# Optimization experiments

Measured on AMD Instinct MI355X. Metric: run time of the kernel, lower is better.

## Reference

```python
import jax, jax.numpy as jnp
import numpy as np

WS = 14  # window size
NH = 12  # num heads
EPS = 1e-5  # torch LayerNorm eps


def _rel_idx(ws: int) -> np.ndarray:
    coords = np.stack(np.meshgrid(np.arange(ws), np.arange(ws), indexing='ij'))
    cf = coords.reshape(2, -1)                      # (2, N)
    rel = cf[:, :, None] - cf[:, None, :]           # (2, N, N)
    rel = rel.transpose(1, 2, 0).copy()
    rel[:, :, 0] += ws - 1
    rel[:, :, 1] += ws - 1
    rel[:, :, 0] *= 2 * ws - 1
    return rel.sum(-1)                              # (N, N) int


def _layernorm(x, w, b):
    mu = jnp.mean(x, axis=-1, keepdims=True)
    var = jnp.var(x, axis=-1, keepdims=True)
    return (x - mu) * jax.lax.rsqrt(var + EPS) * w + b


def setup_inputs() -> dict:
    key = jax.random.key(0)
    ks = jax.random.split(key, 8)
    d, dff = 768, 3072
    s = lambda k, shape, sc: jax.random.normal(k, shape, jnp.float32) * sc
    return {
        'x': jax.random.normal(ks[0], (8, d, 56, 56), jnp.float32),
        'norm1_w': jnp.ones((d,), jnp.float32),
        'norm1_b': jnp.zeros((d,), jnp.float32),
        'qkv_w': s(ks[1], (d, 3 * d), 0.02),
        'qkv_b': jnp.zeros((3 * d,), jnp.float32),
        'rel_bias_table': s(ks[2], ((2 * WS - 1) ** 2, NH), 0.02),
        'proj_w': s(ks[3], (d, d), 0.02),
        'proj_b': jnp.zeros((d,), jnp.float32),
        'norm2_w': jnp.ones((d,), jnp.float32),
        'norm2_b': jnp.zeros((d,), jnp.float32),
        'fc1_w': s(ks[4], (d, dff), 0.02),
        'fc1_b': jnp.zeros((dff,), jnp.float32),
        'fc2_w': s(ks[5], (dff, d), 0.02),
        'fc2_b': jnp.zeros((d,), jnp.float32),
        'gamma1': jnp.full((d,), 1e-5, jnp.float32),
        'gamma2': jnp.full((d,), 1e-5, jnp.float32),
    }


def reference(x, norm1_w, norm1_b, qkv_w, qkv_b, rel_bias_table, proj_w, proj_b,
              norm2_w, norm2_b, fc1_w, fc1_b, fc2_w, fc2_b, gamma1, gamma2):
    B, C, H, W = x.shape
    nh, hd = NH, C // NH
    N = WS * WS
    xs = jnp.transpose(x, (0, 2, 3, 1))             # B,H,W,C
    shortcut = xs
    h = _layernorm(xs, norm1_w, norm1_b)

    # window partition (H, W divisible by WS)
    hw = h.reshape(B, H // WS, WS, W // WS, WS, C)
    hw = jnp.transpose(hw, (0, 1, 3, 2, 4, 5)).reshape(-1, N, C)  # (Bw, N, C)

    qkv = hw @ qkv_w + qkv_b                        # (Bw, N, 3C)
    qkv = qkv.reshape(-1, N, 3, nh, hd)
    q, k, v = [jnp.transpose(qkv[:, :, i], (0, 2, 1, 3)) for i in range(3)]  # (Bw,nh,N,hd)

    attn = jnp.einsum('bhnd,bhmd->bhnm', q, k) * (hd ** -0.5)
    rel_idx = jnp.asarray(_rel_idx(WS))             # static (N,N)
    bias = rel_bias_table[rel_idx]                  # (N,N,nh)
    attn = attn + jnp.transpose(bias, (2, 0, 1))[None]
    attn = jax.nn.softmax(attn, axis=-1)

    out = jnp.einsum('bhnm,bhmd->bnhd', attn, v).reshape(-1, N, C)
    out = out @ proj_w + proj_b                     # (Bw, N, C)

    # window reverse
    out = out.reshape(B, H // WS, W // WS, WS, WS, C)
    out = jnp.transpose(out, (0, 1, 3, 2, 4, 5)).reshape(B, H, W, C)

    xs = shortcut + gamma1 * out
    h2 = _layernorm(xs, norm2_w, norm2_b)
    mlp = jax.nn.gelu(h2 @ fc1_w + fc1_b, approximate=False) @ fc2_w + fc2_b
    xs = xs + gamma2 * mlp
    return jnp.transpose(xs, (0, 3, 1, 2))          # B,C,H,W
```

## Files before the change

### kernel.cpp

```cpp
#include <hip/hip_runtime.h>
#include <cstdint>
#include <cstddef>


typedef unsigned short u16;
typedef short short8 __attribute__((ext_vector_type(8)));
typedef float floatx4 __attribute__((ext_vector_type(4)));

static __device__ __forceinline__ float bf2f(u16 u) {
  return __uint_as_float(((unsigned)u) << 16);
}
static __device__ __forceinline__ u16 f2bf(float f) {
  unsigned u = __float_as_uint(f);
  return (u16)((u + 0x7FFFu + ((u >> 16) & 1u)) >> 16);
}
static __device__ __forceinline__ float ldin(const void* p, size_t i, int isf) {
  return isf ? ((const float*)p)[i] : bf2f(((const u16*)p)[i]);
}
static __device__ __forceinline__ void gload_lds16(const void* g, void* l) {
  __builtin_amdgcn_global_load_lds(
      (const __attribute__((address_space(1))) void*)g,
      (__attribute__((address_space(3))) void*)l, 16, 0, 0);
}
static __device__ __forceinline__ float fast_gelu(float v) {
  float u2 = v * (1.5957691216f + 0.0713548163f * v * v);
  return v * (1.0f / (1.0f + __expf(-u2)));
}

__global__ __launch_bounds__(256) void detect_kernel(const u16* __restrict__ x,
                                                     int* __restrict__ flag) {
  __shared__ int tot;
  if (threadIdx.x == 0) tot = 0;
  __syncthreads();
  int cnt = 0;
  for (int i = threadIdx.x; i < 4096; i += 256) {
    int e = (x[i] >> 7) & 0xFF;
    if (e >= 0xC1) cnt++;
  }
  atomicAdd(&tot, cnt);
  __syncthreads();
  if (threadIdx.x == 0) flag[0] = (tot > 16) ? 1 : 0;
}

__global__ __launch_bounds__(256) void cvt_params_kernel(
    const void* n1w, const void* n1b, const void* qkvb, const void* projb,
    const void* n2w, const void* n2b, const void* fc1b, const void* fc2b,
    const void* g1, const void* g2, const void* bt, u16* __restrict__ P,
    const int* __restrict__ flag) {
  int isf = *flag;
  int i = blockIdx.x * 256 + threadIdx.x;
  const void* src; int off;
  if      (i < 768)   { src = n1w;   off = i; }
  else if (i < 1536)  { src = n1b;   off = i - 768; }
  else if (i < 3840)  { src = qkvb;  off = i - 1536; }
  else if (i < 4608)  { src = projb; off = i - 3840; }
  else if (i < 5376)  { src = n2w;   off = i - 4608; }
  else if (i < 6144)  { src = n2b;   off = i - 5376; }
  else if (i < 9216)  { src = fc1b;  off = i - 6144; }
  else if (i < 9984)  { src = fc2b;  off = i - 9216; }
  else if (i < 10752) { src = g1;    off = i - 9984; }
  else if (i < 11520) { src = g2;    off = i - 10752; }
  else if (i < 20268) { src = bt;    off = i - 11520; }
  else return;
  P[i] = f2bf(ldin(src, off, isf));
}

__global__ __launch_bounds__(256) void wtr_kernel(const void* __restrict__ W,
                                                  u16* __restrict__ WT,
                                                  int K, int N,
                                                  const int* __restrict__ flag) {
  int isf = *flag;
  __shared__ u16 tl[32][33];
  int tx = threadIdx.x, ty = threadIdx.y;
  int n0 = blockIdx.x * 32, k0 = blockIdx.y * 32;
#pragma unroll
  for (int j = 0; j < 32; j += 8)
    tl[ty + j][tx] = f2bf(ldin(W, (size_t)(k0 + ty + j) * N + n0 + tx, isf));
  __syncthreads();
#pragma unroll
  for (int j = 0; j < 32; j += 8)
    WT[(size_t)(n0 + ty + j) * K + k0 + tx] = tl[tx][ty + j];
}

__global__ __launch_bounds__(256) void tin_kernel(const void* __restrict__ x,
                                                  u16* __restrict__ sc,
                                                  const int* __restrict__ flag) {
  int isf = *flag;
  int cc = blockIdx.x, h = blockIdx.y, b = blockIdx.z;
  __shared__ u16 tile[64 * 57];
  int tid = threadIdx.x;
  for (int i = tid; i < 64 * 56; i += 256) {
    int ci = i / 56, w = i - ci * 56;
    tile[ci * 57 + w] =
        f2bf(ldin(x, (((size_t)b * 768 + cc * 64 + ci) * 56 + h) * 56 + w, isf));
  }
  __syncthreads();
  int hb = h / 14, hi = h - hb * 14;
  for (int i = tid; i < 56 * 64; i += 256) {
    int w = i >> 6, ci = i & 63;
    int wb = w / 14, wj = w - wb * 14;
    int r = (b * 16 + hb * 4 + wb) * 196 + hi * 14 + wj;
    sc[(size_t)r * 768 + cc * 64 + ci] = tile[ci * 57 + w];
  }
}

__global__ __launch_bounds__(256) void tout_kernel(const u16* __restrict__ src,
                                                   void* __restrict__ out,
                                                   const int* __restrict__ flag) {
  int isf = *flag;
  int cc = blockIdx.x, h = blockIdx.y, b = blockIdx.z;
  __shared__ u16 tile[64 * 57];
  int tid = threadIdx.x;
  int hb = h / 14, hi = h - hb * 14;
  for (int i = tid; i < 56 * 64; i += 256) {
    int w = i >> 6, ci = i & 63;
    int wb = w / 14, wj = w - wb * 14;
    int r = (b * 16 + hb * 4 + wb) * 196 + hi * 14 + wj;
    tile[ci * 57 + w] = src[(size_t)r * 768 + cc * 64 + ci];
  }
  __syncthreads();
  for (int i = tid; i < 64 * 56; i += 256) {
    int ci = i / 56, w = i - ci * 56;
    size_t o = (((size_t)b * 768 + cc * 64 + ci) * 56 + h) * 56 + w;
    if (isf) ((float*)out)[o] = bf2f(tile[ci * 57 + w]);
    else     ((u16*)out)[o]   = tile[ci * 57 + w];
  }
}

__global__ __launch_bounds__(256) void ln_kernel(const u16* __restrict__ xin,
                                                 const u16* __restrict__ wt,
                                                 const u16* __restrict__ bs,
                                                 u16* __restrict__ out) {
  int row = blockIdx.x, t = threadIdx.x;
  const u16* xr = xin + (size_t)row * 768;
  float v0 = bf2f(xr[t]), v1 = bf2f(xr[t + 256]), v2 = bf2f(xr[t + 512]);
  float s1 = v0 + v1 + v2;
  float s2 = v0 * v0 + v1 * v1 + v2 * v2;
#pragma unroll
  for (int off = 32; off > 0; off >>= 1) {
    s1 += __shfl_xor(s1, off);
    s2 += __shfl_xor(s2, off);
  }
  __shared__ float p1[4], p2[4];
  if ((t & 63) == 0) { p1[t >> 6] = s1; p2[t >> 6] = s2; }
  __syncthreads();
  float S1 = p1[0] + p1[1] + p1[2] + p1[3];
  float S2 = p2[0] + p2[1] + p2[2] + p2[3];
  float mu = S1 * (1.f / 768.f);
  float var = S2 * (1.f / 768.f) - mu * mu;
  float rs = rsqrtf(var + 1e-5f);
  u16* orow = out + (size_t)row * 768;
  orow[t]       = f2bf((v0 - mu) * rs * bf2f(wt[t])       + bf2f(bs[t]));
  orow[t + 256] = f2bf((v1 - mu) * rs * bf2f(wt[t + 256]) + bf2f(bs[t + 256]));
  orow[t + 512] = f2bf((v2 - mu) * rs * bf2f(wt[t + 512]) + bf2f(bs[t + 512]));
}

template <int EPI, int NPH>
__global__ __launch_bounds__(512, 2) void gemm256_kernel(
    const u16* __restrict__ A, const u16* __restrict__ BT,
    const u16* __restrict__ bias, const u16* __restrict__ gamma,
    u16* __restrict__ out, int M, int N, int K, int NX, int NYT) {
  constexpr int BN  = 64 * NPH;
  constexpr int WM  = 8 / NPH;
  constexpr int MF  = 2 * NPH;
  constexpr int ATS = 16384;
  constexpr int BTS = 4096 * NPH;
  __shared__ __align__(16) u16 LDS[2 * ATS + 2 * BTS];

  int bid = blockIdx.x;
  int r8 = bid & 7, q = bid >> 3;
  int xb = q % NX, yb = (q / NX) * 8 + r8;
  if (yb >= NYT) return;
  int m0 = yb * 256, n0 = xb * BN;

  int tid = threadIdx.x;
  int w = tid >> 6, l = tid & 63;
  int l15 = l & 15, quad = l >> 4;
  int wm = w & (WM - 1), wn = w / WM;

  int lrow8 = l >> 3;
  int lk = ((l & 7) ^ lrow8) * 8;
  const u16* aptr[4];
  const u16* bptr[NPH];
#pragma unroll
  for (int j = 0; j < 4; ++j) {
    int ra = m0 + w * 32 + j * 8 + lrow8;
    if (ra > M - 1) ra = M - 1;
    aptr[j] = A + (size_t)ra * K + lk;
  }
#pragma unroll
  for (int j = 0; j < NPH; ++j) {
    int rb = n0 + (w * NPH + j) * 8 + lrow8;
    bptr[j] = BT + (size_t)rb * K + lk;
  }
  int kq0 = (((quad * 16)      ^ ((l15 & 7) << 4)) >> 1);
  int kq1 = (((64 + quad * 16) ^ ((l15 & 7) << 4)) >> 1);

  floatx4 acc[MF][4];
#pragma unroll
  for (int i = 0; i < MF; ++i)
#pragma unroll
    for (int jn = 0; jn < 4; ++jn)
#pragma unroll
      for (int e = 0; e < 4; ++e) acc[i][jn][e] = 0.f;

  int nt = K >> 6;
#pragma unroll
  for (int j = 0; j < 4; ++j)
    gload_lds16(aptr[j], LDS + (w * 4 + j) * 512);
#pragma unroll
  for (int j = 0; j < NPH; ++j)
    gload_lds16(bptr[j], LDS + 2 * ATS + (w * NPH + j) * 512);

  for (int t = 0; t < nt; ++t) {
    int cur = t & 1, nxt = cur ^ 1;
    const u16* Ac = LDS + cur * ATS;
    const u16* Bc = LDS + 2 * ATS + cur * BTS;
    u16* An = LDS + nxt * ATS;
    u16* Bn = LDS + 2 * ATS + nxt * BTS;
    bool pf = (t + 1) < nt;
    int ko = (t + 1) << 6;
    asm volatile("s_waitcnt vmcnt(0)" ::: "memory");
    __builtin_amdgcn_s_barrier();
    short8 bfr[4][2];
#pragma unroll
    for (int p = 0; p < NPH; ++p) {
      if (p == 0) {
#pragma unroll
        for (int ni = 0; ni < 4; ++ni) {
          const u16* bp = Bc + (wn * 64 + ni * 16 + l15) * 64;
          bfr[ni][0] = *(const short8*)(bp + kq0);
          bfr[ni][1] = *(const short8*)(bp + kq1);
        }
      }
      short8 af0[2], af1[2];
      {
        const u16* ap0 = Ac + (wm * (32 * NPH) + (2 * p) * 16 + l15) * 64;
        const u16* ap1 = ap0 + 16 * 64;
        af0[0] = *(const short8*)(ap0 + kq0);
        af0[1] = *(const short8*)(ap0 + kq1);
        af1[0] = *(const short8*)(ap1 + kq0);
        af1[1] = *(const short8*)(ap1 + kq1);
      }
      if (pf) {
        if constexpr (NPH == 4) {
          gload_lds16(aptr[p] + ko, An + (w * 4 + p) * 512);
          gload_lds16(bptr[p] + ko, Bn + (w * 4 + p) * 512);
        } else {
          gload_lds16(aptr[2 * p] + ko,     An + (w * 4 + 2 * p) * 512);
          gload_lds16(aptr[2 * p + 1] + ko, An + (w * 4 + 2 * p + 1) * 512);
          gload_lds16(bptr[p] + ko,         Bn + (w * 2 + p) * 512);
        }
      }
      __builtin_amdgcn_s_barrier();
      __builtin_amdgcn_s_setprio(1);
#pragma unroll
      for (int ni = 0; ni < 4; ++ni) {
        acc[2 * p][ni] = __builtin_amdgcn_mfma_f32_16x16x32_bf16(
            af0[0], bfr[ni][0], acc[2 * p][ni], 0, 0, 0);
        acc[2 * p][ni] = __builtin_amdgcn_mfma_f32_16x16x32_bf16(
            af0[1], bfr[ni][1], acc[2 * p][ni], 0, 0, 0);
        acc[2 * p + 1][ni] = __builtin_amdgcn_mfma_f32_16x16x32_bf16(
            af1[0], bfr[ni][0], acc[2 * p + 1][ni], 0, 0, 0);
        acc[2 * p + 1][ni] = __builtin_amdgcn_mfma_f32_16x16x32_bf16(
            af1[1], bfr[ni][1], acc[2 * p + 1][ni], 0, 0, 0);
      }
      __builtin_amdgcn_s_setprio(0);
      __builtin_amdgcn_s_barrier();
    }
  }

  constexpr int CSTR = BN + 8;
  u16* Cs = LDS;
  float bv[4];
#pragma unroll
  for (int ni = 0; ni < 4; ++ni)
    bv[ni] = bf2f(bias[n0 + wn * 64 + ni * 16 + l15]);
  for (int cch = 0; cch < 2; ++cch) {
    __syncthreads();
    if (((wm * NPH) >> 2) == cch) {
      int rbase = wm * (32 * NPH) - cch * 128 + quad * 4;
#pragma unroll
      for (int mi = 0; mi < MF; ++mi)
#pragma unroll
        for (int ni = 0; ni < 4; ++ni) {
          int cl = wn * 64 + ni * 16 + l15;
#pragma unroll
          for (int reg = 0; reg < 4; ++reg) {
            float v = acc[mi][ni][reg] + bv[ni];
            if constexpr (EPI == 2) v = fast_gelu(v);
            Cs[(rbase + mi * 16 + reg) * CSTR + cl] = f2bf(v);
          }
        }
    }
    __syncthreads();
#pragma unroll
    for (int it = 0; it < BN / 32; ++it) {
      int idx = it * 512 + tid;
      int row = idx / (BN / 8);
      int c8 = (idx - row * (BN / 8)) * 8;
      int grow = m0 + cch * 128 + row;
      if (grow < M) {
        short8 val = *(const short8*)&Cs[row * CSTR + c8];
        u16* po = out + (size_t)grow * N + n0 + c8;
        if constexpr (EPI == 1) {
          short8 rv = *(const short8*)po;
          short8 gv = *(const short8*)(gamma + n0 + c8);
          short8 res;
#pragma unroll
          for (int e = 0; e < 8; ++e)
            res[e] = (short)f2bf(bf2f((u16)rv[e]) +
                                 bf2f((u16)gv[e]) * bf2f((u16)val[e]));
          *(short8*)po = res;
        } else {
          *(short8*)po = val;
        }
      }
    }
  }
}

__global__ __launch_bounds__(256) void attn_kernel(const u16* __restrict__ qkv,
                                                   const u16* __restrict__ btab,
                                                   u16* __restrict__ out) {
  __shared__ __align__(16) u16 VT[64 * 232];
  __shared__ __align__(16) u16 Pa[4 * 2 * 512];
  __shared__ float bS[729];
  int bid = blockIdx.x;
  int win = bid / 12, h = bid - win * 12;
  int tid = threadIdx.x, w = tid >> 6, l = tid & 63;
  int lane15 = l & 15, quad = l >> 4;
  const u16* qbase = qkv + (size_t)win * 196 * 2304;

  for (int i = tid; i < 64 * 28; i += 256) {
    int d = i / 28, m = i - d * 28;
    VT[d * 232 + 196 + m] = 0;
  }
  for (int i = tid; i < 196 * 64; i += 256) {
    int m = i >> 6, d = i & 63;
    VT[d * 232 + m] = qbase[(size_t)m * 2304 + 1536 + h * 64 + d];
  }
  for (int i = tid; i < 729; i += 256) bS[i] = bf2f(btab[i * 12 + h]);
  __syncthreads();

  u16* Pw = Pa + w * 1024;
  for (int rt = w; rt < 13; rt += 4) {
    floatx4 acc[13];
#pragma unroll
    for (int nt = 0; nt < 13; ++nt)
#pragma unroll
      for (int e = 0; e < 4; ++e) acc[nt][e] = 0.f;

    int rq = rt * 16 + lane15;
    bool qok = rq < 196;
#pragma unroll
    for (int kk = 0; kk < 2; ++kk) {
      short8 qf;
      if (qok)
        qf = *(const short8*)&qbase[(size_t)rq * 2304 + h * 64 + kk * 32 + quad * 8];
      else
#pragma unroll
        for (int e = 0; e < 8; ++e) qf[e] = 0;
#pragma unroll
      for (int nt = 0; nt < 13; ++nt) {
        int n = nt * 16 + lane15;
        short8 kf = *(const short8*)&qbase[(size_t)n * 2304 + 768 + h * 64 + kk * 32 + quad * 8];
        acc[nt] = __builtin_amdgcn_mfma_f32_16x16x32_bf16(qf, kf, acc[nt], 0, 0, 0);
      }
    }

    int i1[4], j1[4]; bool rv[4]; float mx[4], sm[4];
#pragma unroll
    for (int reg = 0; reg < 4; ++reg) {
      int r = rt * 16 + quad * 4 + reg;
      i1[reg] = r / 14; j1[reg] = r - i1[reg] * 14;
      rv[reg] = r < 196; mx[reg] = -1e30f; sm[reg] = 0.f;
    }
#pragma unroll
    for (int nt = 0; nt < 13; ++nt) {
      int cc = nt * 16 + lane15;
      bool cv = cc < 196;
      int i2 = cc / 14, j2 = cc - i2 * 14;
#pragma unroll
      for (int reg = 0; reg < 4; ++reg) {
        float v;
        if (cv) {
          v = acc[nt][reg] * 0.125f;
          if (rv[reg]) v += bS[(i1[reg] - i2 + 13) * 27 + (j1[reg] - j2 + 13)];
        } else v = -1e30f;
        acc[nt][reg] = v;
        mx[reg] = fmaxf(mx[reg], v);
      }
    }
#pragma unroll
    for (int reg = 0; reg < 4; ++reg)
#pragma unroll
      for (int off = 1; off < 16; off <<= 1)
        mx[reg] = fmaxf(mx[reg], __shfl_xor(mx[reg], off));
#pragma unroll
    for (int nt = 0; nt < 13; ++nt)
#pragma unroll
      for (int reg = 0; reg < 4; ++reg) {
        float p = __expf(acc[nt][reg] - mx[reg]);
        acc[nt][reg] = p; sm[reg] += p;
      }
#pragma unroll
    for (int reg = 0; reg < 4; ++reg) {
#pragma unroll
      for (int off = 1; off < 16; off <<= 1) sm[reg] += __shfl_xor(sm[reg], off);
      sm[reg] = 1.f / sm[reg];
    }

    floatx4 oa[4];
#pragma unroll
    for (int dt = 0; dt < 4; ++dt)
#pragma unroll
      for (int e = 0; e < 4; ++e) oa[dt][e] = 0.f;
#pragma unroll
    for (int kk = 0; kk < 7; ++kk) {
      u16* Pb = Pw + (kk & 1) * 512;
#pragma unroll
      for (int p = 0; p < 2; ++p) {
        int nt = kk * 2 + p;
#pragma unroll
        for (int reg = 0; reg < 4; ++reg) {
          float v = (nt < 13) ? acc[nt][reg] * sm[reg] : 0.f;
          Pb[(quad * 4 + reg) * 32 + p * 16 + lane15] = f2bf(v);
        }
      }
      asm volatile("s_waitcnt lgkmcnt(0)" ::: "memory");
      short8 pf = *(const short8*)&Pb[lane15 * 32 + quad * 8];
#pragma unroll
      for (int dt = 0; dt < 4; ++dt) {
        short8 vf = *(const short8*)&VT[(dt * 16 + lane15) * 232 + kk * 32 + quad * 8];
        oa[dt] = __builtin_amdgcn_mfma_f32_16x16x32_bf16(pf, vf, oa[dt], 0, 0, 0);
      }
    }
#pragma unroll
    for (int dt = 0; dt < 4; ++dt)
#pragma unroll
      for (int reg = 0; reg < 4; ++reg) {
        int r = rt * 16 + quad * 4 + reg;
        if (r < 196)
          out[((size_t)win * 196 + r) * 768 + h * 64 + dt * 16 + lane15] =
              f2bf(oa[dt][reg]);
      }
  }
}

static inline int gemm_grid(int NX, int NYT) { return NX * ((NYT + 7) / 8) * 8; }

extern "C" void kernel_launch(void* const* d_in, const int* in_sizes, int n_in,
                              void* d_out, int out_size, void* d_ws, size_t ws_size,
                              hipStream_t stream) {
  const void* x      = d_in[0];
  const void* n1w    = d_in[1];
  const void* n1b    = d_in[2];
  const void* qkv_w  = d_in[3];
  const void* qkv_b  = d_in[4];
  const void* btab   = d_in[5];
  const void* proj_w = d_in[6];
  const void* proj_b = d_in[7];
  const void* n2w    = d_in[8];
  const void* n2b    = d_in[9];
  const void* fc1_w  = d_in[10];
  const void* fc1_b  = d_in[11];
  const void* fc2_w  = d_in[12];
  const void* fc2_b  = d_in[13];
  const void* gamma1 = d_in[14];
  const void* gamma2 = d_in[15];
  (void)in_sizes; (void)n_in; (void)out_size;

  int c;
  if      (ws_size >= 245432576ull) c = 1;
  else if (ws_size >= 168362240ull) c = 2;
  else                              c = 4;
  const int R = 25088 / c;
  const int WN = 128 / c;
  const int NYT = (R + 255) / 256;

  char* ws = (char*)d_ws;
  int*  flag  = (int*)ws;
  u16*  P     = (u16*)(ws + 256);
  u16*  qkvT  = (u16*)(ws + 65792);
  u16*  projT = (u16*)(ws + 65792 + 3538944);
  u16*  fc1T  = (u16*)(ws + 65792 + 4718592);
  u16*  fc2T  = (u16*)(ws + 65792 + 9437184);
  const size_t B0 = 38535168;
  u16*  buf0  = (u16*)(ws + 14221568);
  u16*  buf1  = (u16*)(ws + 14221568 + B0);
  char* scr   = ws + 14221568 + 2 * B0;

  u16 *p_n1w = P, *p_n1b = P + 768, *p_qkvb = P + 1536, *p_projb = P + 3840;
  u16 *p_n2w = P + 4608, *p_n2b = P + 5376, *p_fc1b = P + 6144;
  u16 *p_fc2b = P + 9216, *p_g1 = P + 9984, *p_g2 = P + 10752, *p_bt = P + 11520;

  dim3 b256(256), b512(512), bw(32, 8);
  detect_kernel<<<dim3(1), b256, 0, stream>>>((const u16*)x, flag);
  cvt_params_kernel<<<dim3(80), b256, 0, stream>>>(
      n1w, n1b, qkv_b, proj_b, n2w, n2b, fc1_b, fc2_b, gamma1, gamma2, btab,
      P, flag);
  wtr_kernel<<<dim3(72, 24), bw, 0, stream>>>(qkv_w, qkvT, 768, 2304, flag);
  wtr_kernel<<<dim3(24, 24), bw, 0, stream>>>(proj_w, projT, 768, 768, flag);
  wtr_kernel<<<dim3(96, 24), bw, 0, stream>>>(fc1_w, fc1T, 768, 3072, flag);
  wtr_kernel<<<dim3(24, 96), bw, 0, stream>>>(fc2_w, fc2T, 3072, 768, flag);

  tin_kernel<<<dim3(12, 56, 8), b256, 0, stream>>>(x, buf0, flag);
  ln_kernel<<<dim3(25088), b256, 0, stream>>>(buf0, p_n1w, p_n1b, buf1);

  for (int hc = 0; hc < c; ++hc) {
    size_t ro = (size_t)hc * R * 768;
    u16* qC = (u16*)scr;
    u16* aC = (u16*)(scr + (size_t)R * 4608);
    gemm256_kernel<0, 4><<<dim3(gemm_grid(9, NYT)), b512, 0, stream>>>(
        buf1 + ro, qkvT, p_qkvb, nullptr, qC, R, 2304, 768, 9, NYT);
    attn_kernel<<<dim3(WN * 12), b256, 0, stream>>>(qC, p_bt, aC);
    gemm256_kernel<1, 2><<<dim3(gemm_grid(6, NYT)), b512, 0, stream>>>(
        aC, projT, p_projb, p_g1, buf0 + ro, R, 768, 768, 6, NYT);
  }

  ln_kernel<<<dim3(25088), b256, 0, stream>>>(buf0, p_n2w, p_n2b, buf1);

  for (int hc = 0; hc < c; ++hc) {
    size_t ro = (size_t)hc * R * 768;
    u16* gC = (u16*)scr;
    gemm256_kernel<2, 4><<<dim3(gemm_grid(12, NYT)), b512, 0, stream>>>(
        buf1 + ro, fc1T, p_fc1b, nullptr, gC, R, 3072, 768, 12, NYT);
    gemm256_kernel<1, 2><<<dim3(gemm_grid(6, NYT)), b512, 0, stream>>>(
        gC, fc2T, p_fc2b, p_g2, buf0 + ro, R, 768, 3072, 6, NYT);
  }

  tout_kernel<<<dim3(12, 56, 8), b256, 0, stream>>>(buf0, d_out, flag);
}
```

Baseline: 996.4 us.

## Switch GEMM mainloop to 4-stage BK=32 LDS pipeline with partial vmcnt waits

Restructures the 256-row GEMM main loop from a double-buffered BK=64 scheme to a four-buffer ring with BK=32 tiles, prefetching three stages ahead with direct global-to-LDS loads. It waits with partial vmcnt counts instead of draining all outstanding loads, uses one barrier per k-step instead of several, and changes the LDS swizzle to match the narrower tile. The aim is to hide global memory latency better and cut synchronisation overhead. In exchange, each MFMA burst per barrier is smaller and the loop runs twice as many iterations.

```diff
diff --git a/kernel.cpp b/kernel.cpp
--- a/kernel.cpp
+++ b/kernel.cpp
@@ -160,12 +160,13 @@
     const u16* __restrict__ A, const u16* __restrict__ BT,
     const u16* __restrict__ bias, const u16* __restrict__ gamma,
     u16* __restrict__ out, int M, int N, int K, int NX, int NYT) {
-  constexpr int BN  = 64 * NPH;
-  constexpr int WM  = 8 / NPH;
-  constexpr int MF  = 2 * NPH;
-  constexpr int ATS = 16384;
-  constexpr int BTS = 4096 * NPH;
-  __shared__ __align__(16) u16 LDS[2 * ATS + 2 * BTS];
+  constexpr int BN   = 64 * NPH;
+  constexpr int WM   = 8 / NPH;
+  constexpr int MF   = 2 * NPH;
+  constexpr int ABUF = 8192;
+  constexpr int BBUF = 2048 * NPH;
+  constexpr int BUFSZ = ABUF + BBUF;
+  __shared__ __align__(16) u16 LDS[4 * BUFSZ];
 
   int bid = blockIdx.x;
   int r8 = bid & 7, q = bid >> 3;
@@ -178,23 +179,26 @@
   int l15 = l & 15, quad = l >> 4;
   int wm = w & (WM - 1), wn = w / WM;
 
-  int lrow8 = l >> 3;
-  int lk = ((l & 7) ^ lrow8) * 8;
-  const u16* aptr[4];
-  const u16* bptr[NPH];
-#pragma unroll
-  for (int j = 0; j < 4; ++j) {
-    int ra = m0 + w * 32 + j * 8 + lrow8;
-    if (ra > M - 1) ra = M - 1;
-    aptr[j] = A + (size_t)ra * K + lk;
-  }
-#pragma unroll
-  for (int j = 0; j < NPH; ++j) {
-    int rb = n0 + (w * NPH + j) * 8 + lrow8;
-    bptr[j] = BT + (size_t)rb * K + lk;
-  }
-  int kq0 = (((quad * 16)      ^ ((l15 & 7) << 4)) >> 1);
-  int kq1 = (((64 + quad * 16) ^ ((l15 & 7) << 4)) >> 1);
+  int lrow16 = l >> 2;
+  int lk = ((l & 3) ^ ((l >> 3) & 3)) * 8;
+  int ra0 = m0 + w * 32 + lrow16;       if (ra0 > M - 1) ra0 = M - 1;
+  int ra1 = m0 + w * 32 + 16 + lrow16;  if (ra1 > M - 1) ra1 = M - 1;
+  const u16* a0 = A + (size_t)ra0 * K + lk;
+  const u16* a1 = A + (size_t)ra1 * K + lk;
+  const u16* b0;
+  const u16* b1;
+  int dB0, dB1;
+  if constexpr (NPH == 4) {
+    b0 = BT + (size_t)(n0 + w * 32 + lrow16) * K + lk;
+    b1 = BT + (size_t)(n0 + w * 32 + 16 + lrow16) * K + lk;
+    dB0 = (w * 2) * 512; dB1 = (w * 2 + 1) * 512;
+  } else {
+    b0 = BT + (size_t)(n0 + w * 16 + lrow16) * K + lk;
+    b1 = b0; dB0 = w * 512; dB1 = 0;
+  }
+  int dA0 = (w * 2) * 512, dA1 = (w * 2 + 1) * 512;
+
+  int kqs = (quad ^ ((l15 >> 1) & 3)) * 8;
 
   floatx4 acc[MF][4];
 #pragma unroll
@@ -204,70 +208,52 @@
 #pragma unroll
       for (int e = 0; e < 4; ++e) acc[i][jn][e] = 0.f;
 
-  int nt = K >> 6;
-#pragma unroll
-  for (int j = 0; j < 4; ++j)
-    gload_lds16(aptr[j], LDS + (w * 4 + j) * 512);
-#pragma unroll
-  for (int j = 0; j < NPH; ++j)
-    gload_lds16(bptr[j], LDS + 2 * ATS + (w * NPH + j) * 512);
+  int nt = K >> 5;
+
+  auto STAGE = [&](int s) {
+    u16* bb = LDS + (size_t)(s & 3) * BUFSZ;
+    int ko = s << 5;
+    gload_lds16(a0 + ko, bb + dA0);
+    gload_lds16(a1 + ko, bb + dA1);
+    gload_lds16(b0 + ko, bb + ABUF + dB0);
+    if constexpr (NPH == 4) gload_lds16(b1 + ko, bb + ABUF + dB1);
+  };
+
+#pragma unroll
+  for (int pt = 0; pt < 3; ++pt)
+    if (pt < nt) STAGE(pt);
 
   for (int t = 0; t < nt; ++t) {
-    int cur = t & 1, nxt = cur ^ 1;
-    const u16* Ac = LDS + cur * ATS;
-    const u16* Bc = LDS + 2 * ATS + cur * BTS;
-    u16* An = LDS + nxt * ATS;
-    u16* Bn = LDS + 2 * ATS + nxt * BTS;
-    bool pf = (t + 1) < nt;
-    int ko = (t + 1) << 6;
-    asm volatile("s_waitcnt vmcnt(0)" ::: "memory");
+    int rem = nt - 1 - t;
+    if constexpr (NPH == 4) {
+      if (rem >= 2)      asm volatile("s_waitcnt vmcnt(8)" ::: "memory");
+      else if (rem == 1) asm volatile("s_waitcnt vmcnt(4)" ::: "memory");
+      else               asm volatile("s_waitcnt vmcnt(0)" ::: "memory");
+    } else {
+      if (rem >= 2)      asm volatile("s_waitcnt vmcnt(6)" ::: "memory");
+      else if (rem == 1) asm volatile("s_waitcnt vmcnt(3)" ::: "memory");
+      else               asm volatile("s_waitcnt vmcnt(0)" ::: "memory");
+    }
     __builtin_amdgcn_s_barrier();
-    short8 bfr[4][2];
-#pragma unroll
-    for (int p = 0; p < NPH; ++p) {
-      if (p == 0) {
-#pragma unroll
-        for (int ni = 0; ni < 4; ++ni) {
-          const u16* bp = Bc + (wn * 64 + ni * 16 + l15) * 64;
-          bfr[ni][0] = *(const short8*)(bp + kq0);
-          bfr[ni][1] = *(const short8*)(bp + kq1);
-        }
-      }
-      short8 af0[2], af1[2];
-      {
-        const u16* ap0 = Ac + (wm * (32 * NPH) + (2 * p) * 16 + l15) * 64;
-        const u16* ap1 = ap0 + 16 * 64;
-        af0[0] = *(const short8*)(ap0 + kq0);
-        af0[1] = *(const short8*)(ap0 + kq1);
-        af1[0] = *(const short8*)(ap1 + kq0);
-        af1[1] = *(const short8*)(ap1 + kq1);
-      }
-      if (pf) {
-        if constexpr (NPH == 4) {
-          gload_lds16(aptr[p] + ko, An + (w * 4 + p) * 512);
-          gload_lds16(bptr[p] + ko, Bn + (w * 4 + p) * 512);
-        } else {
-          gload_lds16(aptr[2 * p] + ko,     An + (w * 4 + 2 * p) * 512);
-          gload_lds16(aptr[2 * p + 1] + ko, An + (w * 4 + 2 * p + 1) * 512);
-          gload_lds16(bptr[p] + ko,         Bn + (w * 2 + p) * 512);
-        }
-      }
-      __builtin_amdgcn_s_barrier();
-      __builtin_amdgcn_s_setprio(1);
-#pragma unroll
-      for (int ni = 0; ni < 4; ++ni) {
-        acc[2 * p][ni] = __builtin_amdgcn_mfma_f32_16x16x32_bf16(
-            af0[0], bfr[ni][0], acc[2 * p][ni], 0, 0, 0);
-        acc[2 * p][ni] = __builtin_amdgcn_mfma_f32_16x16x32_bf16(
-            af0[1], bfr[ni][1], acc[2 * p][ni], 0, 0, 0);
-        acc[2 * p + 1][ni] = __builtin_amdgcn_mfma_f32_16x16x32_bf16(
-            af1[0], bfr[ni][0], acc[2 * p + 1][ni], 0, 0, 0);
-        acc[2 * p + 1][ni] = __builtin_amdgcn_mfma_f32_16x16x32_bf16(
-            af1[1], bfr[ni][1], acc[2 * p + 1][ni], 0, 0, 0);
-      }
-      __builtin_amdgcn_s_setprio(0);
-      __builtin_amdgcn_s_barrier();
-    }
+    if (t + 3 < nt) STAGE(t + 3);
+
+    const u16* Ac = LDS + (size_t)(t & 3) * BUFSZ;
+    const u16* Bc = Ac + ABUF;
+    __builtin_amdgcn_s_setprio(1);
+    short8 bfr[4];
+#pragma unroll
+    for (int ni = 0; ni < 4; ++ni)
+      bfr[ni] = *(const short8*)&Bc[(wn * 64 + ni * 16 + l15) * 32 + kqs];
+#pragma unroll
+    for (int mi = 0; mi < MF; ++mi) {
+      short8 afr =
+          *(const short8*)&Ac[(wm * (32 * NPH) + mi * 16 + l15) * 32 + kqs];
+#pragma unroll
+      for (int ni = 0; ni < 4; ++ni)
+        acc[mi][ni] = __builtin_amdgcn_mfma_f32_16x16x32_bf16(
+            afr, bfr[ni], acc[mi][ni], 0, 0, 0);
+    }
+    __builtin_amdgcn_s_setprio(0);
   }
 
   constexpr int CSTR = BN + 8;
```

Result: no change. 988.6 us (-0.8%).
